# Performance work log

Hardware: AMD Instinct MI355X
Metric: run time of the kernel (lower is better)

Reference implementation:

```python
import jax, jax.numpy as jnp
import numpy as np

F_BINS, NCH, NSRC, W, H, T, B = 257, 8, 2, 5, 32, 2000, 4
PAD = (W - 1) // 2  # use_pad=True


def setup_inputs() -> dict:
    key = jax.random.key(0)
    ks = jax.random.split(key, 7)
    s = 0.05
    return {
        "x": jax.random.normal(ks[0], (B, 2 * F_BINS, NCH, T), dtype=jnp.float32),
        # per-frequency depthwise complex conv weights: (F, Cout, Cin, w)
        "Wr1": jax.random.normal(ks[1], (F_BINS, H, NCH, W), dtype=jnp.float32) * s,
        "Wi1": jax.random.normal(ks[2], (F_BINS, H, NCH, W), dtype=jnp.float32) * s,
        "Wr2": jax.random.normal(ks[3], (F_BINS, H, H, W), dtype=jnp.float32) * s,
        "Wi2": jax.random.normal(ks[4], (F_BINS, H, H, W), dtype=jnp.float32) * s,
        "Wr3": jax.random.normal(ks[5], (F_BINS, NCH * NSRC, H, W), dtype=jnp.float32) * s,
        "Wi3": jax.random.normal(ks[6], (F_BINS, NCH * NSRC, H, W), dtype=jnp.float32) * s,
    }


def _dwconv(z, Wt):
    # z: (B, F, Cin, T) treated as NCHW with C=F, H=Cin, W=T
    # Wt: (F, Cout, Cin, w) -> grouped conv with groups=F, kernel spans full Cin
    f, cout, cin, w = Wt.shape
    k = Wt.reshape(f * cout, 1, cin, w)
    y = jax.lax.conv_general_dilated(
        z, k, window_strides=(1, 1), padding=[(0, 0), (PAD, PAD)],
        feature_group_count=f, dimension_numbers=("NCHW", "OIHW", "NCHW"))
    b = z.shape[0]
    return y.reshape(b, f, cout, -1)  # (B, F, Cout, T)


def _cconv(zr, zi, Wr, Wi):
    # complex conv: (Wr + i Wi) * (zr + i zi)
    hr = _dwconv(zr, Wr) - _dwconv(zi, Wi)
    hi = _dwconv(zr, Wi) + _dwconv(zi, Wr)
    return hr, hi


def reference(x, Wr1, Wi1, Wr2, Wi2, Wr3, Wi3):
    xr, xi = jnp.split(x, 2, axis=1)  # each (B, F, nCH, T)
    h1r, h1i = _cconv(xr, xi, Wr1, Wi1)
    h1r, h1i = jax.nn.relu(h1r), jax.nn.relu(h1i)
    h2r, h2i = _cconv(h1r, h1i, Wr2, Wi2)
    h2r, h2i = jax.nn.relu(h2r), jax.nn.relu(h2i)
    h3r, h3i = _cconv(h2r, h2i, Wr3, Wi3)  # (B, F, nCH*nSource, T)
    b, f, _, t = xr.shape
    hr = h3r.reshape(b, f, NCH, NSRC, t)
    hi = h3i.reshape(b, f, NCH, NSRC, t)
    # broadcast-multiply and reduce over channels (nCH)
    yrr = jnp.einsum("bfct,bfcst->bfst", xr, hr)
    yri = jnp.einsum("bfct,bfcst->bfst", xr, hi)
    yir = jnp.einsum("bfct,bfcst->bfst", xi, hr)
    yii = jnp.einsum("bfct,bfcst->bfst", xi, hi)
    Yr = yrr - yii
    Yi = yri + yir
    out = jnp.concatenate((Yr, Yi), axis=1)  # (B, 2F, nSource, T); squeeze is a no-op for B>1
    return jnp.squeeze(out)
```

## Files before the change

### kernel.cpp

```cpp
#include <hip/hip_runtime.h>

#define F_BINS 257
#define NCH    8
#define NSRC   2
#define KW     5
#define HCH    32
#define TLEN   2000
#define BATCH  4

#define TT      128
#define NTILES  16
#define NK      (BATCH * F_BINS)
#define NRANK   ((NK + 7) / 8)
#define GRID    (NRANK * NTILES * 8)

#define XSTRIDE 24
#define XCOLS   148
#define HWIN    144
#define HSZ     (HWIN * 64 * 2)
#define H1OFF   0
#define XOFF    HSZ
#define H2OFF   HSZ
#define H3OFF   0
#define SMEM_BYTES (2 * HSZ)
#define H3STRIDE 40

#define NFRAG   36
#define PW_HALF8_PER_F (NFRAG * 2 * 64)
#define PW_BYTES ((size_t)F_BINS * PW_HALF8_PER_F * 16)

typedef _Float16 half8  __attribute__((ext_vector_type(8)));
typedef __fp16   pk16x2 __attribute__((ext_vector_type(2)));
typedef __fp16   pk16x4 __attribute__((ext_vector_type(4)));
typedef float    f32x4  __attribute__((ext_vector_type(4)));

#define MFMA16(a, b, c) __builtin_amdgcn_mfma_f32_16x16x32_f16(a, b, c, 0, 0, 0)

__device__ __forceinline__ half8 gather_frag(
    int f, int frag, int mw, int lane,
    const float* __restrict__ Wr1, const float* __restrict__ Wi1,
    const float* __restrict__ Wr2, const float* __restrict__ Wi2,
    const float* __restrict__ Wr3, const float* __restrict__ Wi3)
{
    const int g = lane >> 4, r16 = lane & 15;
    half8 v;
    if (frag < 6) {
        int hr = frag / 3, p = frag % 3;
        int tap = 2 * p + (g >> 1);
        #pragma unroll
        for (int j = 0; j < 8; ++j) {
            float val = 0.f;
            if (tap < KW) {
                long idx = (((long)f * HCH + hr * 16 + r16) * NCH + j) * KW + tap;
                if (mw == 0) val = (g & 1) ? -Wi1[idx] : Wr1[idx];
                else         val = (g & 1) ?  Wr1[idx] : Wi1[idx];
            }
            v[j] = (_Float16)val;
        }
    } else if (frag < 26) {
        int u = frag - 6;
        int w = u >> 2, hr = (u >> 1) & 1, kk = u & 1;
        #pragma unroll
        for (int j = 0; j < 8; ++j) {
            int c = g * 8 + j;
            long idx = (((long)f * HCH + hr * 16 + r16) * HCH + c) * KW + w;
            float val;
            if (mw == 0) val = kk ? -Wi2[idx] : Wr2[idx];
            else         val = kk ?  Wr2[idx] : Wi2[idx];
            v[j] = (_Float16)val;
        }
    } else {
        int u = frag - 26;
        int w = u >> 1, kk = u & 1;
        #pragma unroll
        for (int j = 0; j < 8; ++j) {
            int c = g * 8 + j;
            long idx = (((long)f * (NCH * NSRC) + r16) * HCH + c) * KW + w;
            float val;
            if (mw == 0) val = kk ? -Wi3[idx] : Wr3[idx];
            else         val = kk ?  Wr3[idx] : Wi3[idx];
            v[j] = (_Float16)val;
        }
    }
    return v;
}

__global__ __launch_bounds__(256) void repack_kernel(
    const float* __restrict__ Wr1, const float* __restrict__ Wi1,
    const float* __restrict__ Wr2, const float* __restrict__ Wi2,
    const float* __restrict__ Wr3, const float* __restrict__ Wi3,
    _Float16* __restrict__ pw)
{
    const int bid  = blockIdx.x;
    const int f    = bid >> 2;
    const int part = bid & 3;
    const int lane = threadIdx.x & 63;
    const int q    = threadIdx.x >> 6;
    half8* pwv = (half8*)pw;
    for (int u = part * 18 + q; u < part * 18 + 18; u += 4) {
        int frag = u >> 1, mw = u & 1;
        half8 v = gather_frag(f, frag, mw, lane, Wr1, Wi1, Wr2, Wi2, Wr3, Wi3);
        pwv[((size_t)f * (NFRAG * 2) + u) * 64 + lane] = v;
    }
}

template<bool PACKED>
__global__ __launch_bounds__(256, 4) void cddcnn_mfma_kernel(
    const float* __restrict__ x,
    const float* __restrict__ Wr1, const float* __restrict__ Wi1,
    const float* __restrict__ Wr2, const float* __restrict__ Wi2,
    const float* __restrict__ Wr3, const float* __restrict__ Wi3,
    float* __restrict__ out, const _Float16* __restrict__ pw)
{
    __shared__ __align__(16) char sm[SMEM_BYTES];

    const int tid  = threadIdx.x;
    const int lane = tid & 63;
    const int wv   = tid >> 6;
    const int mw   = wv >> 1;
    const int nw   = wv & 1;
    const int g    = lane >> 4;
    const int r16  = lane & 15;

    const int bid  = blockIdx.x;
    const int xcd  = bid & 7;
    const int rt   = bid >> 3;
    const int tl   = rt & 15;
    const int k    = ((rt >> 4) << 3) | xcd;
    if (k >= NK) return;
    const int f    = k % F_BINS;
    const int b    = k / F_BINS;
    const int t0   = tl * TT;
    const bool interior = (tl >= 1) && (tl <= 14);

    const int nb0 = nw ? 5 : 0;
    const int nbn = nw ? 4 : 5;

    const half8* pwf = PACKED ? ((const half8*)pw) + (size_t)f * PW_HALF8_PER_F + mw * 64 + lane
                              : nullptr;
    #define LOADFRAG(fr) (PACKED ? pwf[(fr) * 128] \
                                 : gather_frag(f, (fr), mw, lane, Wr1, Wi1, Wr2, Wi2, Wr3, Wi3))

    const long xr_base = ((long)(b * 2 * F_BINS + f) * NCH) * TLEN;
    const long xi_base = ((long)(b * 2 * F_BINS + F_BINS + f) * NCH) * TLEN;

    half8 pkr = {}, pki = {};
    if (tid < XCOLS) {
        int t = t0 - 10 + tid;
        bool ok = (t >= 0) && (t < TLEN);
        #pragma unroll
        for (int c = 0; c < 8; ++c) {
            float vr = ok ? x[xr_base + (long)c * TLEN + t] : 0.f;
            float vi = ok ? x[xi_base + (long)c * TLEN + t] : 0.f;
            pkr[c] = (_Float16)vr;
            pki[c] = (_Float16)vi;
        }
        *(half8*)(sm + XOFF + tid * (XSTRIDE * 2))      = pkr;
        *(half8*)(sm + XOFF + tid * (XSTRIDE * 2) + 16) = pki;
    }

    half8 a1[2][3];
    #pragma unroll
    for (int hr = 0; hr < 2; ++hr)
    #pragma unroll
    for (int p = 0; p < 3; ++p)
        a1[hr][p] = LOADFRAG(hr * 3 + p);
    __syncthreads();

    const int Xc = (r16 & 7) << 4;
    int woff64[2];
    #pragma unroll
    for (int hr = 0; hr < 2; ++hr)
        woff64[hr] = ((mw * 64 + hr * 32 + g * 8) ^ Xc);

    half8 a2n[2][2];

    {
        f32x4 acc[2][5] = {};
        const char* xb = sm + XOFF + ((nb0 * 16 + r16) * XSTRIDE + (g & 1) * 8) * 2;
        #pragma unroll
        for (int p = 0; p < 3; ++p) {
            int tap = 2 * p + (g >> 1);
            if (tap > 4) tap = 4;
            const char* xbp = xb + tap * (XSTRIDE * 2);
            #pragma unroll
            for (int nbi = 0; nbi < 5; ++nbi) {
                if (nbi < nbn) {
                    const half8 bf = *(const half8*)(xbp + nbi * (16 * XSTRIDE * 2));
                    acc[0][nbi] = MFMA16(a1[0][p], bf, acc[0][nbi]);
                    acc[1][nbi] = MFMA16(a1[1][p], bf, acc[1][nbi]);
                }
            }
        }

        #pragma unroll
        for (int hr = 0; hr < 2; ++hr)
        #pragma unroll
        for (int kk = 0; kk < 2; ++kk)
            a2n[hr][kk] = LOADFRAG(6 + hr * 2 + kk);

        char* wb = sm + H1OFF + (nb0 * 16 + r16) * 128;
        #pragma unroll
        for (int nbi = 0; nbi < 5; ++nbi) {
            if (nbi < nbn) {
                int t = t0 - 8 + nb0 * 16 + r16 + nbi * 16;
                bool ok = interior || ((t >= 0) && (t < TLEN));
                #pragma unroll
                for (int hr = 0; hr < 2; ++hr) {
                    float v0 = ok ? fmaxf(acc[hr][nbi][0], 0.f) : 0.f;
                    float v1 = ok ? fmaxf(acc[hr][nbi][1], 0.f) : 0.f;
                    float v2 = ok ? fmaxf(acc[hr][nbi][2], 0.f) : 0.f;
                    float v3 = ok ? fmaxf(acc[hr][nbi][3], 0.f) : 0.f;
                    pk16x2 lo = __builtin_amdgcn_cvt_pkrtz(v0, v1);
                    pk16x2 hi = __builtin_amdgcn_cvt_pkrtz(v2, v3);
                    pk16x4 hv; hv[0] = lo[0]; hv[1] = lo[1]; hv[2] = hi[0]; hv[3] = hi[1];
                    *(pk16x4*)(wb + nbi * 2048 + woff64[hr]) = hv;
                }
            }
        }
    }
    __syncthreads();

    {
        f32x4 acc[2][5] = {};
        #pragma unroll
        for (int w = 0; w < KW; ++w) {
            half8 a2c[2][2];
            #pragma unroll
            for (int hr = 0; hr < 2; ++hr)
            #pragma unroll
            for (int kk = 0; kk < 2; ++kk)
                a2c[hr][kk] = a2n[hr][kk];
            if (w < 4) {
                #pragma unroll
                for (int hr = 0; hr < 2; ++hr)
                #pragma unroll
                for (int kk = 0; kk < 2; ++kk)
                    a2n[hr][kk] = LOADFRAG(6 + (w + 1) * 4 + hr * 2 + kk);
            }

            const int sc0 = nb0 * 16 + r16 + w - 2;
            const int vb  = sc0 * 128 + ((g * 16) ^ ((sc0 & 7) << 4));
            #pragma unroll
            for (int kk = 0; kk < 2; ++kk) {
                const char* rb = sm + H1OFF + (kk ? (vb ^ 64) : vb);
                #pragma unroll
                for (int nbi = 0; nbi < 5; ++nbi) {
                    if (nbi < nbn) {
                        const half8 bf = *(const half8*)(rb + nbi * 2048);
                        acc[0][nbi] = MFMA16(a2c[0][kk], bf, acc[0][nbi]);
                        acc[1][nbi] = MFMA16(a2c[1][kk], bf, acc[1][nbi]);
                    }
                }
            }
        }

        #pragma unroll
        for (int kk = 0; kk < 2; ++kk)
            a2n[0][kk] = LOADFRAG(26 + kk);

        char* wb = sm + H2OFF + (nb0 * 16 + r16) * 128;
        #pragma unroll
        for (int nbi = 0; nbi < 5; ++nbi) {
            if (nbi < nbn) {
                int t = t0 - 8 + nb0 * 16 + r16 + nbi * 16;
                bool ok = interior || ((t >= 0) && (t < TLEN));
                #pragma unroll
                for (int hr = 0; hr < 2; ++hr) {
                    float v0 = ok ? fmaxf(acc[hr][nbi][0], 0.f) : 0.f;
                    float v1 = ok ? fmaxf(acc[hr][nbi][1], 0.f) : 0.f;
                    float v2 = ok ? fmaxf(acc[hr][nbi][2], 0.f) : 0.f;
                    float v3 = ok ? fmaxf(acc[hr][nbi][3], 0.f) : 0.f;
                    pk16x2 lo = __builtin_amdgcn_cvt_pkrtz(v0, v1);
                    pk16x2 hi = __builtin_amdgcn_cvt_pkrtz(v2, v3);
                    pk16x4 hv; hv[0] = lo[0]; hv[1] = lo[1]; hv[2] = hi[0]; hv[3] = hi[1];
                    *(pk16x4*)(wb + nbi * 2048 + woff64[hr]) = hv;
                }
            }
        }
    }
    __syncthreads();

    {
        f32x4 acc3[4] = {};
        #pragma unroll
        for (int w = 0; w < KW; ++w) {
            half8 a3c[2];
            #pragma unroll
            for (int kk = 0; kk < 2; ++kk)
                a3c[kk] = a2n[0][kk];
            if (w < 4) {
                #pragma unroll
                for (int kk = 0; kk < 2; ++kk)
                    a2n[0][kk] = LOADFRAG(26 + (w + 1) * 2 + kk);
            }

            const int sc0 = nw * 64 + r16 + 6 + w;
            const int vb  = sc0 * 128 + ((g * 16) ^ ((sc0 & 7) << 4));
            #pragma unroll
            for (int kk = 0; kk < 2; ++kk) {
                const char* rb = sm + H2OFF + (kk ? (vb ^ 64) : vb);
                #pragma unroll
                for (int nbi = 0; nbi < 4; ++nbi) {
                    const half8 bf = *(const half8*)(rb + nbi * 2048);
                    acc3[nbi] = MFMA16(a3c[kk], bf, acc3[nbi]);
                }
            }
        }
        char* wb3 = sm + H3OFF + (nw * 64 + r16) * (H3STRIDE * 2) + mw * 32 + g * 8;
        #pragma unroll
        for (int nbi = 0; nbi < 4; ++nbi) {
            pk16x2 lo = __builtin_amdgcn_cvt_pkrtz(acc3[nbi][0], acc3[nbi][1]);
            pk16x2 hi = __builtin_amdgcn_cvt_pkrtz(acc3[nbi][2], acc3[nbi][3]);
            pk16x4 hv; hv[0] = lo[0]; hv[1] = lo[1]; hv[2] = hi[0]; hv[3] = hi[1];
            *(pk16x4*)(wb3 + nbi * (16 * H3STRIDE * 2)) = hv;
        }
    }
    __syncthreads();

    {
        int col = tid - 10;
        if (col >= 0 && col < TT) {
            int t = t0 + col;
            if (t < TLEN) {
                half8 h3q[4];
                #pragma unroll
                for (int q = 0; q < 4; ++q)
                    h3q[q] = *(const half8*)(sm + H3OFF + col * (H3STRIDE * 2) + q * 16);
                float Yr[2] = {0.f, 0.f}, Yi[2] = {0.f, 0.f};
                #pragma unroll
                for (int c = 0; c < NCH; ++c) {
                    float vr = (float)pkr[c];
                    float vi = (float)pki[c];
                    #pragma unroll
                    for (int s = 0; s < NSRC; ++s) {
                        int o = 2 * c + s;
                        float hr = (c < 4) ? (float)h3q[0][o] : (float)h3q[1][o - 8];
                        float hi = (c < 4) ? (float)h3q[2][o] : (float)h3q[3][o - 8];
                        Yr[s] += vr * hr - vi * hi;
                        Yi[s] += vr * hi + vi * hr;
                    }
                }
                #pragma unroll
                for (int s = 0; s < NSRC; ++s) {
                    out[((long)(b * 2 * F_BINS + f) * NSRC + s) * TLEN + t]          = Yr[s];
                    out[((long)(b * 2 * F_BINS + F_BINS + f) * NSRC + s) * TLEN + t] = Yi[s];
                }
            }
        }
    }
}

extern "C" void kernel_launch(void* const* d_in, const int* in_sizes, int n_in,
                              void* d_out, int out_size, void* d_ws, size_t ws_size,
                              hipStream_t stream) {
    const float* x   = (const float*)d_in[0];
    const float* Wr1 = (const float*)d_in[1];
    const float* Wi1 = (const float*)d_in[2];
    const float* Wr2 = (const float*)d_in[3];
    const float* Wi2 = (const float*)d_in[4];
    const float* Wr3 = (const float*)d_in[5];
    const float* Wi3 = (const float*)d_in[6];
    float* out = (float*)d_out;

    dim3 block(256);
    dim3 grid(GRID);
    if (ws_size >= PW_BYTES) {
        _Float16* pw = (_Float16*)d_ws;
        repack_kernel<<<F_BINS * 4, block, 0, stream>>>(Wr1, Wi1, Wr2, Wi2, Wr3, Wi3, pw);
        cddcnn_mfma_kernel<true><<<grid, block, 0, stream>>>(
            x, Wr1, Wi1, Wr2, Wi2, Wr3, Wi3, out, pw);
    } else {
        cddcnn_mfma_kernel<false><<<grid, block, 0, stream>>>(
            x, Wr1, Wi1, Wr2, Wi2, Wr3, Wi3, out, nullptr);
    }
}
```

Measured before the change: 237.6 us.

## Shrink time tiles and split waves by columns instead of output rows

```diff
diff --git a/kernel.cpp b/kernel.cpp
--- a/kernel.cpp
+++ b/kernel.cpp
@@ -8,15 +8,15 @@
 #define TLEN   2000
 #define BATCH  4
 
-#define TT      128
-#define NTILES  16
+#define TT      112
+#define NTILES  18
 #define NK      (BATCH * F_BINS)
 #define NRANK   ((NK + 7) / 8)
 #define GRID    (NRANK * NTILES * 8)
 
 #define XSTRIDE 24
-#define XCOLS   148
-#define HWIN    144
+#define XCOLS   132
+#define HWIN    128
 #define HSZ     (HWIN * 64 * 2)
 #define H1OFF   0
 #define XOFF    HSZ
@@ -117,29 +117,26 @@
     const int tid  = threadIdx.x;
     const int lane = tid & 63;
     const int wv   = tid >> 6;
-    const int mw   = wv >> 1;
-    const int nw   = wv & 1;
     const int g    = lane >> 4;
     const int r16  = lane & 15;
 
     const int bid  = blockIdx.x;
     const int xcd  = bid & 7;
     const int rt   = bid >> 3;
-    const int tl   = rt & 15;
-    const int k    = ((rt >> 4) << 3) | xcd;
+    const int tl   = rt % NTILES;
+    const int k    = (rt / NTILES) * 8 + xcd;
     if (k >= NK) return;
     const int f    = k % F_BINS;
     const int b    = k / F_BINS;
     const int t0   = tl * TT;
-    const bool interior = (tl >= 1) && (tl <= 14);
-
-    const int nb0 = nw ? 5 : 0;
-    const int nbn = nw ? 4 : 5;
-
-    const half8* pwf = PACKED ? ((const half8*)pw) + (size_t)f * PW_HALF8_PER_F + mw * 64 + lane
+    const bool interior = (tl >= 1) && (tl <= 16);
+
+    const int colb = wv * 32 + r16;
+
+    const half8* pwb = PACKED ? ((const half8*)pw) + (size_t)f * PW_HALF8_PER_F + lane
                               : nullptr;
-    #define LOADFRAG(fr) (PACKED ? pwf[(fr) * 128] \
-                                 : gather_frag(f, (fr), mw, lane, Wr1, Wi1, Wr2, Wi2, Wr3, Wi3))
+    #define LOADFRAG2(fr, mww) (PACKED ? pwb[((fr) * 2 + (mww)) * 64] \
+                  : gather_frag(f, (fr), (mww), lane, Wr1, Wi1, Wr2, Wi2, Wr3, Wi3))
 
     const long xr_base = ((long)(b * 2 * F_BINS + f) * NCH) * TLEN;
     const long xi_base = ((long)(b * 2 * F_BINS + F_BINS + f) * NCH) * TLEN;
@@ -159,161 +156,191 @@
         *(half8*)(sm + XOFF + tid * (XSTRIDE * 2) + 16) = pki;
     }
 
-    half8 a1[2][3];
+    half8 a1[2][2][3];
+    #pragma unroll
+    for (int mw = 0; mw < 2; ++mw)
     #pragma unroll
     for (int hr = 0; hr < 2; ++hr)
     #pragma unroll
     for (int p = 0; p < 3; ++p)
-        a1[hr][p] = LOADFRAG(hr * 3 + p);
+        a1[mw][hr][p] = LOADFRAG2(hr * 3 + p, mw);
     __syncthreads();
 
     const int Xc = (r16 & 7) << 4;
-    int woff64[2];
+    int woff64[2][2];
+    #pragma unroll
+    for (int mw = 0; mw < 2; ++mw)
     #pragma unroll
     for (int hr = 0; hr < 2; ++hr)
-        woff64[hr] = ((mw * 64 + hr * 32 + g * 8) ^ Xc);
-
-    half8 a2n[2][2];
+        woff64[mw][hr] = ((mw * 64 + hr * 32 + g * 8) ^ Xc);
+
+    half8 a2n[2][2][2];
 
     {
-        f32x4 acc[2][5] = {};
-        const char* xb = sm + XOFF + ((nb0 * 16 + r16) * XSTRIDE + (g & 1) * 8) * 2;
+        f32x4 acc[2][2][2] = {};
+        const char* xb = sm + XOFF + (colb * XSTRIDE + (g & 1) * 8) * 2;
         #pragma unroll
         for (int p = 0; p < 3; ++p) {
             int tap = 2 * p + (g >> 1);
             if (tap > 4) tap = 4;
             const char* xbp = xb + tap * (XSTRIDE * 2);
             #pragma unroll
-            for (int nbi = 0; nbi < 5; ++nbi) {
-                if (nbi < nbn) {
-                    const half8 bf = *(const half8*)(xbp + nbi * (16 * XSTRIDE * 2));
-                    acc[0][nbi] = MFMA16(a1[0][p], bf, acc[0][nbi]);
-                    acc[1][nbi] = MFMA16(a1[1][p], bf, acc[1][nbi]);
-                }
-            }
-        }
-
+            for (int cbi = 0; cbi < 2; ++cbi) {
+                const half8 bf = *(const half8*)(xbp + cbi * (16 * XSTRIDE * 2));
+                #pragma unroll
+                for (int mw = 0; mw < 2; ++mw)
+                #pragma unroll
+                for (int hr = 0; hr < 2; ++hr)
+                    acc[cbi][mw][hr] = MFMA16(a1[mw][hr][p], bf, acc[cbi][mw][hr]);
+            }
+        }
+
+        #pragma unroll
+        for (int mw = 0; mw < 2; ++mw)
         #pragma unroll
         for (int hr = 0; hr < 2; ++hr)
         #pragma unroll
         for (int kk = 0; kk < 2; ++kk)
-            a2n[hr][kk] = LOADFRAG(6 + hr * 2 + kk);
-
-        char* wb = sm + H1OFF + (nb0 * 16 + r16) * 128;
-        #pragma unroll
-        for (int nbi = 0; nbi < 5; ++nbi) {
-            if (nbi < nbn) {
-                int t = t0 - 8 + nb0 * 16 + r16 + nbi * 16;
-                bool ok = interior || ((t >= 0) && (t < TLEN));
-                #pragma unroll
-                for (int hr = 0; hr < 2; ++hr) {
-                    float v0 = ok ? fmaxf(acc[hr][nbi][0], 0.f) : 0.f;
-                    float v1 = ok ? fmaxf(acc[hr][nbi][1], 0.f) : 0.f;
-                    float v2 = ok ? fmaxf(acc[hr][nbi][2], 0.f) : 0.f;
-                    float v3 = ok ? fmaxf(acc[hr][nbi][3], 0.f) : 0.f;
-                    pk16x2 lo = __builtin_amdgcn_cvt_pkrtz(v0, v1);
-                    pk16x2 hi = __builtin_amdgcn_cvt_pkrtz(v2, v3);
-                    pk16x4 hv; hv[0] = lo[0]; hv[1] = lo[1]; hv[2] = hi[0]; hv[3] = hi[1];
-                    *(pk16x4*)(wb + nbi * 2048 + woff64[hr]) = hv;
-                }
+            a2n[mw][hr][kk] = LOADFRAG2(6 + hr * 2 + kk, mw);
+
+        char* wb = sm + H1OFF + colb * 128;
+        #pragma unroll
+        for (int cbi = 0; cbi < 2; ++cbi) {
+            int t = t0 - 8 + colb + cbi * 16;
+            bool ok = interior || ((t >= 0) && (t < TLEN));
+            #pragma unroll
+            for (int mw = 0; mw < 2; ++mw)
+            #pragma unroll
+            for (int hr = 0; hr < 2; ++hr) {
+                float v0 = ok ? fmaxf(acc[cbi][mw][hr][0], 0.f) : 0.f;
+                float v1 = ok ? fmaxf(acc[cbi][mw][hr][1], 0.f) : 0.f;
+                float v2 = ok ? fmaxf(acc[cbi][mw][hr][2], 0.f) : 0.f;
+                float v3 = ok ? fmaxf(acc[cbi][mw][hr][3], 0.f) : 0.f;
+                pk16x2 lo = __builtin_amdgcn_cvt_pkrtz(v0, v1);
+                pk16x2 hi = __builtin_amdgcn_cvt_pkrtz(v2, v3);
+                pk16x4 hv; hv[0] = lo[0]; hv[1] = lo[1]; hv[2] = hi[0]; hv[3] = hi[1];
+                *(pk16x4*)(wb + cbi * 2048 + woff64[mw][hr]) = hv;
             }
         }
     }
     __syncthreads();
 
+    half8 a3n[2][2];
+
     {
-        f32x4 acc[2][5] = {};
+        f32x4 acc[2][2][2] = {};
         #pragma unroll
         for (int w = 0; w < KW; ++w) {
-            half8 a2c[2][2];
+            half8 a2c[2][2][2];
+            #pragma unroll
+            for (int mw = 0; mw < 2; ++mw)
             #pragma unroll
             for (int hr = 0; hr < 2; ++hr)
             #pragma unroll
             for (int kk = 0; kk < 2; ++kk)
-                a2c[hr][kk] = a2n[hr][kk];
+                a2c[mw][hr][kk] = a2n[mw][hr][kk];
             if (w < 4) {
                 #pragma unroll
+                for (int mw = 0; mw < 2; ++mw)
+                #pragma unroll
                 for (int hr = 0; hr < 2; ++hr)
                 #pragma unroll
                 for (int kk = 0; kk < 2; ++kk)
-                    a2n[hr][kk] = LOADFRAG(6 + (w + 1) * 4 + hr * 2 + kk);
-            }
-
-            const int sc0 = nb0 * 16 + r16 + w - 2;
+                    a2n[mw][hr][kk] = LOADFRAG2(6 + (w + 1) * 4 + hr * 2 + kk, mw);
+            }
+
+            const int sc0 = colb + w - 2;
             const int vb  = sc0 * 128 + ((g * 16) ^ ((sc0 & 7) << 4));
             #pragma unroll
             for (int kk = 0; kk < 2; ++kk) {
                 const char* rb = sm + H1OFF + (kk ? (vb ^ 64) : vb);
                 #pragma unroll
-                for (int nbi = 0; nbi < 5; ++nbi) {
-                    if (nbi < nbn) {
-                        const half8 bf = *(const half8*)(rb + nbi * 2048);
-                        acc[0][nbi] = MFMA16(a2c[0][kk], bf, acc[0][nbi]);
-                        acc[1][nbi] = MFMA16(a2c[1][kk], bf, acc[1][nbi]);
+                for (int cbi = 0; cbi < 2; ++cbi) {
+                    const half8 bf = *(const half8*)(rb + cbi * 2048);
+                    #pragma unroll
+                    for (int mw = 0; mw < 2; ++mw)
+                    #pragma unroll
+                    for (int hr = 0; hr < 2; ++hr)
+                        acc[cbi][mw][hr] = MFMA16(a2c[mw][hr][kk], bf, acc[cbi][mw][hr]);
+                }
+            }
+        }
+
+        #pragma unroll
+        for (int mw = 0; mw < 2; ++mw)
+        #pragma unroll
+        for (int kk = 0; kk < 2; ++kk)
+            a3n[mw][kk] = LOADFRAG2(26 + kk, mw);
+
+        char* wb = sm + H2OFF + colb * 128;
+        #pragma unroll
+        for (int cbi = 0; cbi < 2; ++cbi) {
+            int t = t0 - 8 + colb + cbi * 16;
+            bool ok = interior || ((t >= 0) && (t < TLEN));
+            #pragma unroll
+            for (int mw = 0; mw < 2; ++mw)
+            #pragma unroll
+            for (int hr = 0; hr < 2; ++hr) {
+                float v0 = ok ? fmaxf(acc[cbi][mw][hr][0], 0.f) : 0.f;
+                float v1 = ok ? fmaxf(acc[cbi][mw][hr][1], 0.f) : 0.f;
+                float v2 = ok ? fmaxf(acc[cbi][mw][hr][2], 0.f) : 0.f;
+                float v3 = ok ? fmaxf(acc[cbi][mw][hr][3], 0.f) : 0.f;
+                pk16x2 lo = __builtin_amdgcn_cvt_pkrtz(v0, v1);
+                pk16x2 hi = __builtin_amdgcn_cvt_pkrtz(v2, v3);
+                pk16x4 hv; hv[0] = lo[0]; hv[1] = lo[1]; hv[2] = hi[0]; hv[3] = hi[1];
+                *(pk16x4*)(wb + cbi * 2048 + woff64[mw][hr]) = hv;
+            }
+        }
+    }
+    __syncthreads();
+
+    {
+        const int ncb3 = (wv == 3) ? 1 : 2;
+        f32x4 acc3[2][2] = {};
+        #pragma unroll
+        for (int w = 0; w < KW; ++w) {
+            half8 a3c[2][2];
+            #pragma unroll
+            for (int mw = 0; mw < 2; ++mw)
+            #pragma unroll
+            for (int kk = 0; kk < 2; ++kk)
+                a3c[mw][kk] = a3n[mw][kk];
+            if (w < 4) {
+                #pragma unroll
+                for (int mw = 0; mw < 2; ++mw)
+                #pragma unroll
+                for (int kk = 0; kk < 2; ++kk)
+                    a3n[mw][kk] = LOADFRAG2(26 + (w + 1) * 2 + kk, mw);
+            }
+
+            const int sc0 = colb + 6 + w;
+            const int vb  = sc0 * 128 + ((g * 16) ^ ((sc0 & 7) << 4));
+            #pragma unroll
+            for (int kk = 0; kk < 2; ++kk) {
+                const char* rb = sm + H2OFF + (kk ? (vb ^ 64) : vb);
+                #pragma unroll
+                for (int cbi = 0; cbi < 2; ++cbi) {
+                    if (cbi < ncb3) {
+                        const half8 bf = *(const half8*)(rb + cbi * 2048);
+                        #pragma unroll
+                        for (int mw = 0; mw < 2; ++mw)
+                            acc3[cbi][mw] = MFMA16(a3c[mw][kk], bf, acc3[cbi][mw]);
                     }
                 }
             }
         }
-
-        #pragma unroll
-        for (int kk = 0; kk < 2; ++kk)
-            a2n[0][kk] = LOADFRAG(26 + kk);
-
-        char* wb = sm + H2OFF + (nb0 * 16 + r16) * 128;
-        #pragma unroll
-        for (int nbi = 0; nbi < 5; ++nbi) {
-            if (nbi < nbn) {
-                int t = t0 - 8 + nb0 * 16 + r16 + nbi * 16;
-                bool ok = interior || ((t >= 0) && (t < TLEN));
-                #pragma unroll
-                for (int hr = 0; hr < 2; ++hr) {
-                    float v0 = ok ? fmaxf(acc[hr][nbi][0], 0.f) : 0.f;
-                    float v1 = ok ? fmaxf(acc[hr][nbi][1], 0.f) : 0.f;
-                    float v2 = ok ? fmaxf(acc[hr][nbi][2], 0.f) : 0.f;
-                    float v3 = ok ? fmaxf(acc[hr][nbi][3], 0.f) : 0.f;
-                    pk16x2 lo = __builtin_amdgcn_cvt_pkrtz(v0, v1);
-                    pk16x2 hi = __builtin_amdgcn_cvt_pkrtz(v2, v3);
+        char* wb3 = sm + H3OFF + colb * (H3STRIDE * 2) + g * 8;
+        #pragma unroll
+        for (int cbi = 0; cbi < 2; ++cbi) {
+            if (cbi < ncb3) {
+                #pragma unroll
+                for (int mw = 0; mw < 2; ++mw) {
+                    pk16x2 lo = __builtin_amdgcn_cvt_pkrtz(acc3[cbi][mw][0], acc3[cbi][mw][1]);
+                    pk16x2 hi = __builtin_amdgcn_cvt_pkrtz(acc3[cbi][mw][2], acc3[cbi][mw][3]);
                     pk16x4 hv; hv[0] = lo[0]; hv[1] = lo[1]; hv[2] = hi[0]; hv[3] = hi[1];
-                    *(pk16x4*)(wb + nbi * 2048 + woff64[hr]) = hv;
+                    *(pk16x4*)(wb3 + cbi * (16 * H3STRIDE * 2) + mw * 32) = hv;
                 }
             }
-        }
-    }
-    __syncthreads();
-
-    {
-        f32x4 acc3[4] = {};
-        #pragma unroll
-        for (int w = 0; w < KW; ++w) {
-            half8 a3c[2];
-            #pragma unroll
-            for (int kk = 0; kk < 2; ++kk)
-                a3c[kk] = a2n[0][kk];
-            if (w < 4) {
-                #pragma unroll
-                for (int kk = 0; kk < 2; ++kk)
-                    a2n[0][kk] = LOADFRAG(26 + (w + 1) * 2 + kk);
-            }
-
-            const int sc0 = nw * 64 + r16 + 6 + w;
-            const int vb  = sc0 * 128 + ((g * 16) ^ ((sc0 & 7) << 4));
-            #pragma unroll
-            for (int kk = 0; kk < 2; ++kk) {
-                const char* rb = sm + H2OFF + (kk ? (vb ^ 64) : vb);
-                #pragma unroll
-                for (int nbi = 0; nbi < 4; ++nbi) {
-                    const half8 bf = *(const half8*)(rb + nbi * 2048);
-                    acc3[nbi] = MFMA16(a3c[kk], bf, acc3[nbi]);
-                }
-            }
-        }
-        char* wb3 = sm + H3OFF + (nw * 64 + r16) * (H3STRIDE * 2) + mw * 32 + g * 8;
-        #pragma unroll
-        for (int nbi = 0; nbi < 4; ++nbi) {
-            pk16x2 lo = __builtin_amdgcn_cvt_pkrtz(acc3[nbi][0], acc3[nbi][1]);
-            pk16x2 hi = __builtin_amdgcn_cvt_pkrtz(acc3[nbi][2], acc3[nbi][3]);
-            pk16x4 hv; hv[0] = lo[0]; hv[1] = lo[1]; hv[2] = hi[0]; hv[3] = hi[1];
-            *(pk16x4*)(wb3 + nbi * (16 * H3STRIDE * 2)) = hv;
         }
     }
     __syncthreads();
```

Result: slower. 268.0 us (+12.8%).
